# Optimization experiments

Measured on AMD Instinct MI355X. Metric: run time of the kernel, lower is better.

The kernel has to match this reference:

```python
import jax, jax.numpy as jnp
import numpy as np

S = 7
STEP = 1.0 / S
LAMBDA_COORD = 5.0
LAMBDA_NOOBJ = 0.5


def setup_inputs() -> dict:
    key = jax.random.key(0)
    k1, k2, k3 = jax.random.split(key, 3)
    B = 16384
    pred = jax.random.uniform(k1, (B, S, S, 30), dtype=jnp.float32)
    target = jax.random.uniform(k2, (B, S, S, 30), dtype=jnp.float32)
    conf = (jax.random.uniform(k3, (B, S, S)) > 0.9).astype(jnp.float32)
    target = target.at[..., 4].set(conf)
    return {"pred": pred, "target": target}


def _convert_box(box):
    # box: [..., S, S, 4] in cell-relative (x, y, w, h); returns clipped corners.
    gi = jnp.arange(S, dtype=box.dtype).reshape(1, S, 1)  # first spatial axis -> x offset
    gj = jnp.arange(S, dtype=box.dtype).reshape(1, 1, S)  # second spatial axis -> y offset
    x, y, w, h = box[..., 0], box[..., 1], box[..., 2], box[..., 3]
    cx = (x + gi) * STEP
    cy = (y + gj) * STEP
    x1 = jnp.maximum(cx - w / 2, 0.0)
    y1 = jnp.maximum(cy - h / 2, 0.0)
    x2 = jnp.minimum(cx + w / 2, 1.0)
    y2 = jnp.minimum(cy + h / 2, 1.0)
    return x1, y1, x2, y2


def _iou(b1, b2):
    a, b, c, d = b1
    q, w, e, r = b2
    minx = jnp.maximum(a, q)
    miny = jnp.maximum(b, w)
    maxx = jnp.minimum(c, e)
    maxy = jnp.minimum(d, r)
    inter = (maxy - miny) * (maxx - minx)  # faithful: no clamping of negative overlaps
    union = (e - q) * (r - w) + (d - b) * (c - a) - inter
    return jnp.where(inter > 0, inter / (union + 1e-05), 0.0)


def reference(pred, target):
    B = pred.shape[0]
    tbox = _convert_box(target[..., :4])
    pbox1 = _convert_box(pred[..., 0:4])
    pbox2 = _convert_box(pred[..., 5:9])
    iou1 = _iou(tbox, pbox1)  # [B, S, S]
    iou2 = _iou(tbox, pbox2)

    sel2 = iou1 <= iou2  # original: box1 responsible only if iou1 > iou2
    conf_t = jax.lax.stop_gradient(jnp.where(sel2, iou2, iou1))  # .item() detached iou
    pxy = jnp.where(sel2[..., None], pred[..., 5:7], pred[..., 0:2])
    pwh = jnp.where(sel2[..., None], pred[..., 7:9], pred[..., 2:4])
    pconf = jnp.where(sel2, pred[..., 9], pred[..., 4])

    obj = (target[..., 4] > 0).astype(pred.dtype)  # [B, S, S]
    noobj = (target[..., 4] == 0).astype(pred.dtype)

    obj_loss = jnp.sum(obj * (pconf - conf_t) ** 2)
    xy_loss = jnp.sum(obj[..., None] * (pxy - target[..., 0:2]) ** 2)
    wh_loss = jnp.sum(obj[..., None] * (pwh - target[..., 2:4]) ** 2)
    class_loss = jnp.sum(obj[..., None] * (pred[..., 10:] - target[..., 10:]) ** 2)
    noobj_loss = jnp.sum(noobj * ((pred[..., 4] - target[..., 4]) ** 2 + (pred[..., 9] - target[..., 9]) ** 2))

    loss = obj_loss + LAMBDA_NOOBJ * noobj_loss + LAMBDA_COORD * (xy_loss + wh_loss) + class_loss
    return loss / B
```

## Files before the change

### kernel.cpp

```cpp
#include <hip/hip_runtime.h>


#define NS 7
#define NC 30

__global__ void zero_out_kernel(float* out) { out[0] = 0.0f; }

__global__ __launch_bounds__(256) void yolo_loss_kernel(
    const float* __restrict__ pred,
    const float* __restrict__ targ,
    float* __restrict__ out,
    int n_cells, float inv_B)
{
    const float STEP = 1.0f / 7.0f;
    const float L_COORD = 5.0f;
    const float L_NOOBJ = 0.5f;

    int cell = blockIdx.x * blockDim.x + threadIdx.x;
    float lsum = 0.0f;
    if (cell < n_cells) {
        int j = cell % NS;
        int i = (cell / NS) % NS;
        float gi = (float)i;
        float gj = (float)j;

        const float2* p2 = (const float2*)pred + (size_t)cell * 15;
        const float2* t2 = (const float2*)targ + (size_t)cell * 15;
        float p[NC], t[NC];
        #pragma unroll
        for (int k = 0; k < 15; ++k) {
            float2 v = p2[k]; p[2 * k] = v.x; p[2 * k + 1] = v.y;
        }
        #pragma unroll
        for (int k = 0; k < 15; ++k) {
            float2 u = t2[k]; t[2 * k] = u.x; t[2 * k + 1] = u.y;
        }

        float ta, tb, tc, td;
        {
            float cx = (t[0] + gi) * STEP;
            float cy = (t[1] + gj) * STEP;
            ta = fmaxf(cx - t[2] * 0.5f, 0.0f);
            tb = fmaxf(cy - t[3] * 0.5f, 0.0f);
            tc = fminf(cx + t[2] * 0.5f, 1.0f);
            td = fminf(cy + t[3] * 0.5f, 1.0f);
        }
        float q1, w1, e1, r1;
        {
            float cx = (p[0] + gi) * STEP;
            float cy = (p[1] + gj) * STEP;
            q1 = fmaxf(cx - p[2] * 0.5f, 0.0f);
            w1 = fmaxf(cy - p[3] * 0.5f, 0.0f);
            e1 = fminf(cx + p[2] * 0.5f, 1.0f);
            r1 = fminf(cy + p[3] * 0.5f, 1.0f);
        }
        float q2, w2, e2, r2;
        {
            float cx = (p[5] + gi) * STEP;
            float cy = (p[6] + gj) * STEP;
            q2 = fmaxf(cx - p[7] * 0.5f, 0.0f);
            w2 = fmaxf(cy - p[8] * 0.5f, 0.0f);
            e2 = fminf(cx + p[7] * 0.5f, 1.0f);
            r2 = fminf(cy + p[8] * 0.5f, 1.0f);
        }

        float tarea = (td - tb) * (tc - ta);
        float iou1, iou2;
        {
            float minx = fmaxf(ta, q1), miny = fmaxf(tb, w1);
            float maxx = fminf(tc, e1), maxy = fminf(td, r1);
            float inter = (maxy - miny) * (maxx - minx);
            float uni = (e1 - q1) * (r1 - w1) + tarea - inter;
            iou1 = (inter > 0.0f) ? inter / (uni + 1e-5f) : 0.0f;
        }
        {
            float minx = fmaxf(ta, q2), miny = fmaxf(tb, w2);
            float maxx = fminf(tc, e2), maxy = fminf(td, r2);
            float inter = (maxy - miny) * (maxx - minx);
            float uni = (e2 - q2) * (r2 - w2) + tarea - inter;
            iou2 = (inter > 0.0f) ? inter / (uni + 1e-5f) : 0.0f;
        }

        bool sel2 = (iou1 <= iou2);
        float conf_t = sel2 ? iou2 : iou1;
        float px = sel2 ? p[5] : p[0];
        float py = sel2 ? p[6] : p[1];
        float pw = sel2 ? p[7] : p[2];
        float ph = sel2 ? p[8] : p[3];
        float pconf = sel2 ? p[9] : p[4];

        float obj = (t[4] > 0.0f) ? 1.0f : 0.0f;
        float noobj = (t[4] == 0.0f) ? 1.0f : 0.0f;

        float dx = px - t[0], dy = py - t[1];
        float dw = pw - t[2], dh = ph - t[3];
        float coord = dx * dx + dy * dy + dw * dw + dh * dh;

        float dc = pconf - conf_t;
        float obj_loss = dc * dc;

        float cls = 0.0f;
        #pragma unroll
        for (int k = 10; k < NC; ++k) {
            float d = p[k] - t[k];
            cls += d * d;
        }

        float d4 = p[4] - t[4];
        float d9 = p[9] - t[9];
        float noobj_loss = d4 * d4 + d9 * d9;

        lsum = obj * (obj_loss + L_COORD * coord + cls) + L_NOOBJ * noobj * noobj_loss;
    }

    #pragma unroll
    for (int off = 32; off > 0; off >>= 1)
        lsum += __shfl_down(lsum, off, 64);

    __shared__ float wsum[4];
    int lane = threadIdx.x & 63;
    int wid = threadIdx.x >> 6;
    if (lane == 0) wsum[wid] = lsum;
    __syncthreads();
    if (threadIdx.x == 0) {
        float s = (wsum[0] + wsum[1]) + (wsum[2] + wsum[3]);
        atomicAdd(out, s * inv_B);
    }
}

extern "C" void kernel_launch(void* const* d_in, const int* in_sizes, int n_in,
                              void* d_out, int out_size, void* d_ws, size_t ws_size,
                              hipStream_t stream) {
    const float* pred = (const float*)d_in[0];
    const float* targ = (const float*)d_in[1];
    float* out = (float*)d_out;

    const int B = 16384;
    const int n_cells = B * NS * NS;
    const float inv_B = 1.0f / (float)B;

    zero_out_kernel<<<1, 1, 0, stream>>>(out);

    const int block = 256;
    const int grid = (n_cells + block - 1) / block;
    yolo_loss_kernel<<<grid, block, 0, stream>>>(pred, targ, out, n_cells, inv_B);
}
```

Measured before the change: 204.3 us.

## Process two cells per thread with float4 loads and two-pass reduction

Each thread now handles a pair of adjacent cells, loading 60 floats per tensor with float4 vector loads instead of float2. The grid size is hardcoded from the pair count. When workspace is available, per-block partial sums go to workspace and a second single-block kernel reduces them, replacing the global atomic and the separate zero kernel. The 120-float register arrays raise register pressure and may cut occupancy, and the hardcoded sizes drop bounds checks.

After: 211.3 us. 1.03x slower.

```diff
diff --git a/kernel.cpp b/kernel.cpp
--- a/kernel.cpp
+++ b/kernel.cpp
@@ -3,129 +3,164 @@
 
 #define NS 7
 #define NC 30
+#define BLOCK 256
+#define NPAIRS 401408
+#define GRID (NPAIRS / BLOCK)
 
 __global__ void zero_out_kernel(float* out) { out[0] = 0.0f; }
 
-__global__ __launch_bounds__(256) void yolo_loss_kernel(
-    const float* __restrict__ pred,
-    const float* __restrict__ targ,
-    float* __restrict__ out,
-    int n_cells, float inv_B)
+__device__ __forceinline__ float cell_loss(const float* __restrict__ p,
+                                           const float* __restrict__ t,
+                                           float gi, float gj)
 {
     const float STEP = 1.0f / 7.0f;
     const float L_COORD = 5.0f;
     const float L_NOOBJ = 0.5f;
 
-    int cell = blockIdx.x * blockDim.x + threadIdx.x;
-    float lsum = 0.0f;
-    if (cell < n_cells) {
-        int j = cell % NS;
-        int i = (cell / NS) % NS;
-        float gi = (float)i;
-        float gj = (float)j;
+    float ta, tb, tc, td;
+    {
+        float cx = (t[0] + gi) * STEP;
+        float cy = (t[1] + gj) * STEP;
+        ta = fmaxf(cx - t[2] * 0.5f, 0.0f);
+        tb = fmaxf(cy - t[3] * 0.5f, 0.0f);
+        tc = fminf(cx + t[2] * 0.5f, 1.0f);
+        td = fminf(cy + t[3] * 0.5f, 1.0f);
+    }
+    float q1, w1, e1, r1;
+    {
+        float cx = (p[0] + gi) * STEP;
+        float cy = (p[1] + gj) * STEP;
+        q1 = fmaxf(cx - p[2] * 0.5f, 0.0f);
+        w1 = fmaxf(cy - p[3] * 0.5f, 0.0f);
+        e1 = fminf(cx + p[2] * 0.5f, 1.0f);
+        r1 = fminf(cy + p[3] * 0.5f, 1.0f);
+    }
+    float q2, w2, e2, r2;
+    {
+        float cx = (p[5] + gi) * STEP;
+        float cy = (p[6] + gj) * STEP;
+        q2 = fmaxf(cx - p[7] * 0.5f, 0.0f);
+        w2 = fmaxf(cy - p[8] * 0.5f, 0.0f);
+        e2 = fminf(cx + p[7] * 0.5f, 1.0f);
+        r2 = fminf(cy + p[8] * 0.5f, 1.0f);
+    }
 
-        const float2* p2 = (const float2*)pred + (size_t)cell * 15;
-        const float2* t2 = (const float2*)targ + (size_t)cell * 15;
-        float p[NC], t[NC];
-        #pragma unroll
-        for (int k = 0; k < 15; ++k) {
-            float2 v = p2[k]; p[2 * k] = v.x; p[2 * k + 1] = v.y;
-        }
-        #pragma unroll
-        for (int k = 0; k < 15; ++k) {
-            float2 u = t2[k]; t[2 * k] = u.x; t[2 * k + 1] = u.y;
-        }
+    float tarea = (td - tb) * (tc - ta);
+    float iou1, iou2;
+    {
+        float minx = fmaxf(ta, q1), miny = fmaxf(tb, w1);
+        float maxx = fminf(tc, e1), maxy = fminf(td, r1);
+        float inter = (maxy - miny) * (maxx - minx);
+        float uni = (e1 - q1) * (r1 - w1) + tarea - inter;
+        iou1 = (inter > 0.0f) ? inter / (uni + 1e-5f) : 0.0f;
+    }
+    {
+        float minx = fmaxf(ta, q2), miny = fmaxf(tb, w2);
+        float maxx = fminf(tc, e2), maxy = fminf(td, r2);
+        float inter = (maxy - miny) * (maxx - minx);
+        float uni = (e2 - q2) * (r2 - w2) + tarea - inter;
+        iou2 = (inter > 0.0f) ? inter / (uni + 1e-5f) : 0.0f;
+    }
 
-        float ta, tb, tc, td;
-        {
-            float cx = (t[0] + gi) * STEP;
-            float cy = (t[1] + gj) * STEP;
-            ta = fmaxf(cx - t[2] * 0.5f, 0.0f);
-            tb = fmaxf(cy - t[3] * 0.5f, 0.0f);
-            tc = fminf(cx + t[2] * 0.5f, 1.0f);
-            td = fminf(cy + t[3] * 0.5f, 1.0f);
-        }
-        float q1, w1, e1, r1;
-        {
-            float cx = (p[0] + gi) * STEP;
-            float cy = (p[1] + gj) * STEP;
-            q1 = fmaxf(cx - p[2] * 0.5f, 0.0f);
-            w1 = fmaxf(cy - p[3] * 0.5f, 0.0f);
-            e1 = fminf(cx + p[2] * 0.5f, 1.0f);
-            r1 = fminf(cy + p[3] * 0.5f, 1.0f);
-        }
-        float q2, w2, e2, r2;
-        {
-            float cx = (p[5] + gi) * STEP;
-            float cy = (p[6] + gj) * STEP;
-            q2 = fmaxf(cx - p[7] * 0.5f, 0.0f);
-            w2 = fmaxf(cy - p[8] * 0.5f, 0.0f);
-            e2 = fminf(cx + p[7] * 0.5f, 1.0f);
-            r2 = fminf(cy + p[8] * 0.5f, 1.0f);
-        }
+    bool sel2 = (iou1 <= iou2);
+    float conf_t = sel2 ? iou2 : iou1;
+    float px = sel2 ? p[5] : p[0];
+    float py = sel2 ? p[6] : p[1];
+    float pw = sel2 ? p[7] : p[2];
+    float ph = sel2 ? p[8] : p[3];
+    float pconf = sel2 ? p[9] : p[4];
 
-        float tarea = (td - tb) * (tc - ta);
-        float iou1, iou2;
-        {
-            float minx = fmaxf(ta, q1), miny = fmaxf(tb, w1);
-            float maxx = fminf(tc, e1), maxy = fminf(td, r1);
-            float inter = (maxy - miny) * (maxx - minx);
-            float uni = (e1 - q1) * (r1 - w1) + tarea - inter;
-            iou1 = (inter > 0.0f) ? inter / (uni + 1e-5f) : 0.0f;
-        }
-        {
-            float minx = fmaxf(ta, q2), miny = fmaxf(tb, w2);
-            float maxx = fminf(tc, e2), maxy = fminf(td, r2);
-            float inter = (maxy - miny) * (maxx - minx);
-            float uni = (e2 - q2) * (r2 - w2) + tarea - inter;
-            iou2 = (inter > 0.0f) ? inter / (uni + 1e-5f) : 0.0f;
-        }
+    float obj = (t[4] > 0.0f) ? 1.0f : 0.0f;
+    float noobj = (t[4] == 0.0f) ? 1.0f : 0.0f;
 
-        bool sel2 = (iou1 <= iou2);
-        float conf_t = sel2 ? iou2 : iou1;
-        float px = sel2 ? p[5] : p[0];
-        float py = sel2 ? p[6] : p[1];
-        float pw = sel2 ? p[7] : p[2];
-        float ph = sel2 ? p[8] : p[3];
-        float pconf = sel2 ? p[9] : p[4];
+    float dx = px - t[0], dy = py - t[1];
+    float dw = pw - t[2], dh = ph - t[3];
+    float coord = dx * dx + dy * dy + dw * dw + dh * dh;
 
-        float obj = (t[4] > 0.0f) ? 1.0f : 0.0f;
-        float noobj = (t[4] == 0.0f) ? 1.0f : 0.0f;
+    float dc = pconf - conf_t;
+    float obj_loss = dc * dc;
 
-        float dx = px - t[0], dy = py - t[1];
-        float dw = pw - t[2], dh = ph - t[3];
-        float coord = dx * dx + dy * dy + dw * dw + dh * dh;
+    float cls = 0.0f;
+    #pragma unroll
+    for (int k = 10; k < NC; ++k) {
+        float d = p[k] - t[k];
+        cls += d * d;
+    }
 
-        float dc = pconf - conf_t;
-        float obj_loss = dc * dc;
+    float d4 = p[4] - t[4];
+    float d9 = p[9] - t[9];
+    float noobj_loss = d4 * d4 + d9 * d9;
 
-        float cls = 0.0f;
-        #pragma unroll
-        for (int k = 10; k < NC; ++k) {
-            float d = p[k] - t[k];
-            cls += d * d;
-        }
+    return obj * (obj_loss + L_COORD * coord + cls) + L_NOOBJ * noobj * noobj_loss;
+}
 
-        float d4 = p[4] - t[4];
-        float d9 = p[9] - t[9];
-        float noobj_loss = d4 * d4 + d9 * d9;
+__global__ __launch_bounds__(BLOCK) void yolo_loss_main(
+    const float* __restrict__ pred,
+    const float* __restrict__ targ,
+    float* __restrict__ partial,
+    float* __restrict__ out,
+    int atomic_mode, float inv_B)
+{
+    const int tid = threadIdx.x;
+    const int u = blockIdx.x * BLOCK + tid;
 
-        lsum = obj * (obj_loss + L_COORD * coord + cls) + L_NOOBJ * noobj * noobj_loss;
+    float fp[60], ft[60];
+    const float4* pg = (const float4*)pred + (size_t)u * 15;
+    const float4* tg = (const float4*)targ + (size_t)u * 15;
+    #pragma unroll
+    for (int k = 0; k < 15; ++k) {
+        float4 v = pg[k];
+        fp[4 * k] = v.x; fp[4 * k + 1] = v.y; fp[4 * k + 2] = v.z; fp[4 * k + 3] = v.w;
     }
+    #pragma unroll
+    for (int k = 0; k < 15; ++k) {
+        float4 v = tg[k];
+        ft[4 * k] = v.x; ft[4 * k + 1] = v.y; ft[4 * k + 2] = v.z; ft[4 * k + 3] = v.w;
+    }
+
+    const int cellA = 2 * u;
+    const int cellB = 2 * u + 1;
+    const int jA = cellA % NS, iA = (cellA / NS) % NS;
+    const int jB = cellB % NS, iB = (cellB / NS) % NS;
+
+    float lsum = cell_loss(fp, ft, (float)iA, (float)jA)
+               + cell_loss(fp + 30, ft + 30, (float)iB, (float)jB);
 
     #pragma unroll
     for (int off = 32; off > 0; off >>= 1)
         lsum += __shfl_down(lsum, off, 64);
 
     __shared__ float wsum[4];
-    int lane = threadIdx.x & 63;
-    int wid = threadIdx.x >> 6;
+    int lane = tid & 63;
+    int wid = tid >> 6;
     if (lane == 0) wsum[wid] = lsum;
     __syncthreads();
-    if (threadIdx.x == 0) {
+    if (tid == 0) {
         float s = (wsum[0] + wsum[1]) + (wsum[2] + wsum[3]);
-        atomicAdd(out, s * inv_B);
+        if (atomic_mode) atomicAdd(out, s * inv_B);
+        else partial[blockIdx.x] = s;
     }
+}
+
+__global__ __launch_bounds__(BLOCK) void reduce_kernel(
+    const float* __restrict__ partial, float* __restrict__ out,
+    int n, float inv_B)
+{
+    const int tid = threadIdx.x;
+    float s = 0.0f;
+    for (int idx = tid; idx < n; idx += BLOCK) s += partial[idx];
+
+    #pragma unroll
+    for (int off = 32; off > 0; off >>= 1)
+        s += __shfl_down(s, off, 64);
+
+    __shared__ float wsum[4];
+    int lane = tid & 63;
+    int wid = tid >> 6;
+    if (lane == 0) wsum[wid] = s;
+    __syncthreads();
+    if (tid == 0)
+        out[0] = ((wsum[0] + wsum[1]) + (wsum[2] + wsum[3])) * inv_B;
 }
 
 extern "C" void kernel_launch(void* const* d_in, const int* in_sizes, int n_in,
@@ -136,12 +171,14 @@
     float* out = (float*)d_out;
 
     const int B = 16384;
-    const int n_cells = B * NS * NS;
     const float inv_B = 1.0f / (float)B;
 
-    zero_out_kernel<<<1, 1, 0, stream>>>(out);
-
-    const int block = 256;
-    const int grid = (n_cells + block - 1) / block;
-    yolo_loss_kernel<<<grid, block, 0, stream>>>(pred, targ, out, n_cells, inv_B);
+    if (ws_size >= GRID * sizeof(float) && d_ws != nullptr) {
+        float* partial = (float*)d_ws;
+        yolo_loss_main<<<GRID, BLOCK, 0, stream>>>(pred, targ, partial, out, 0, inv_B);
+        reduce_kernel<<<1, BLOCK, 0, stream>>>(partial, out, GRID, inv_B);
+    } else {
+        zero_out_kernel<<<1, 1, 0, stream>>>(out);
+        yolo_loss_main<<<GRID, BLOCK, 0, stream>>>(pred, targ, nullptr, out, 1, inv_B);
+    }
 }
```
